# Optimization experiments

Measured on AMD Instinct MI355X. Metric: run time of the kernel, lower is better.

Reference implementation:

```python
import jax, jax.numpy as jnp
import numpy as np

B, L, D, H = 4, 2048, 1024, 16
DH = D // H  # 64
MASK_VALUE = -1000000.0
EPS = 1e-12


def setup_inputs() -> dict:
    key = jax.random.key(0)
    ks = jax.random.split(key, 7)
    s = 1.0 / np.sqrt(D)
    x = jax.random.normal(ks[0], (B, L, D), dtype=jnp.float32)
    Wq = jax.random.uniform(ks[1], (D, H * DH), jnp.float32, -s, s)
    Wk = jax.random.uniform(ks[2], (D, H * DH), jnp.float32, -s, s)
    Wv = jax.random.uniform(ks[3], (D, H * DH), jnp.float32, -s, s)
    Wo = jax.random.uniform(ks[4], (H * DH, D), jnp.float32, -s, s)
    gamma = jnp.ones((D,), jnp.float32)
    beta = jnp.zeros((D,), jnp.float32)
    # causal mask: True positions are masked (query m cannot attend to key n > m)
    attn_mask = jnp.triu(jnp.ones((L, L), dtype=bool), k=1)
    return {"x": x, "Wq": Wq, "Wk": Wk, "Wv": Wv, "Wo": Wo,
            "gamma": gamma, "beta": beta, "attn_mask": attn_mask}


def _layernorm(y, gamma, beta):
    mu = jnp.mean(y, axis=-1, keepdims=True)
    var = jnp.mean(jnp.square(y - mu), axis=-1, keepdims=True)
    return (y - mu) * jax.lax.rsqrt(var + EPS) * gamma + beta


def reference(x, Wq, Wk, Wv, Wo, gamma, beta, attn_mask):
    scale = 1.0 / np.sqrt(DH)
    # projections, reshape to heads: B L (H D) -> B H L D
    q = (x @ Wq).reshape(B, L, H, DH).transpose(0, 2, 1, 3)
    k = (x @ Wk).reshape(B, L, H, DH).transpose(0, 2, 1, 3)
    v = (x @ Wv).reshape(B, L, H, DH).transpose(0, 2, 1, 3)
    scores = jnp.einsum('bhmd,bhnd->bhmn', q, k) * scale
    scores = jnp.where(attn_mask, MASK_VALUE, scores)
    probs = jax.nn.softmax(scores, axis=-1)
    z = jnp.einsum('bhmn,bhnd->bhmd', probs, v)
    z = z.transpose(0, 2, 1, 3).reshape(B, L, H * DH)
    out = jax.nn.relu(z @ Wo)
    return _layernorm(out + x, gamma, beta)
```

## Files before the change

### kernel.cpp

```cpp
#include <hip/hip_runtime.h>
#include <math.h>

#define B_ 4
#define L_ 2048
#define D_ 1024
#define H_ 16
#define DH_ 64
#define QKV_N 3072

typedef unsigned short ushort_t;
typedef unsigned int uint_t;
using bf16x8 = __attribute__((ext_vector_type(8))) short;
using f32x4  = __attribute__((ext_vector_type(4))) float;

__device__ __forceinline__ ushort_t f2bf(float f) {
    union { float f; unsigned int u; } v; v.f = f;
    unsigned int u = v.u;
    unsigned int rnd = ((u >> 16) & 1u) + 0x7fffu;
    return (ushort_t)((u + rnd) >> 16);
}

__device__ __forceinline__ float bf2f(ushort_t u) {
    union { unsigned int u; float f; } v;
    v.u = ((unsigned int)u) << 16;
    return v.f;
}

__device__ __forceinline__ void glds16(const void* g, void* l) {
    __builtin_amdgcn_global_load_lds(
        (const __attribute__((address_space(1))) unsigned int*)g,
        (__attribute__((address_space(3))) unsigned int*)l, 16, 0, 0);
}

__global__ __launch_bounds__(256) void prep(const float* __restrict__ Wq,
                                            const float* __restrict__ Wk,
                                            const float* __restrict__ Wv,
                                            const float* __restrict__ Wo,
                                            const float* __restrict__ x,
                                            ushort_t* __restrict__ wcat,
                                            ushort_t* __restrict__ wto,
                                            ushort_t* __restrict__ xb) {
    const int t = threadIdx.x;
    if (blockIdx.z == 4) {
        const int bid = blockIdx.y * 16 + blockIdx.x;
        const int base = bid * 32768 + t * 4;
        #pragma unroll
        for (int it = 0; it < 32; ++it) {
            float4 v = *(const float4*)(x + base + it * 1024);
            ushort4 o;
            o.x = f2bf(v.x); o.y = f2bf(v.y); o.z = f2bf(v.z); o.w = f2bf(v.w);
            *(ushort4*)(xb + base + it * 1024) = o;
        }
        return;
    }
    __shared__ ushort_t tile[64][65];
    const int widx = blockIdx.z;
    const float* W = (widx == 0) ? Wq : (widx == 1) ? Wk : (widx == 2) ? Wv : Wo;
    ushort_t* dst = (widx < 3) ? (wcat + (size_t)widx * 1024 * 1024) : wto;
    const int j = t & 63, i0 = t >> 6;
    const int kbase = blockIdx.y * 64, nbase = blockIdx.x * 64;
    #pragma unroll
    for (int it = 0; it < 16; ++it) {
        int i = it * 4 + i0;
        tile[i][j] = f2bf(W[(size_t)(kbase + i) * 1024 + nbase + j]);
    }
    __syncthreads();
    #pragma unroll
    for (int it = 0; it < 16; ++it) {
        int nn = it * 4 + i0;
        dst[(size_t)(nbase + nn) * 1024 + kbase + j] = tile[j][nn];
    }
}

__global__ __launch_bounds__(256) void gemm_mfma(const ushort_t* __restrict__ A,
                                                 const ushort_t* __restrict__ Wt,
                                                 ushort_t* __restrict__ Cbf,
                                                 const ushort_t* __restrict__ resid,
                                                 int M, int N, int K, int fuse) {
    __shared__ ushort_t As[128 * 64];
    __shared__ ushort_t Bs[128 * 64];
    const int t = threadIdx.x;
    const int w = t >> 6, ln = t & 63;
    const int l15 = ln & 15, quad = ln >> 4;
    const int bm = blockIdx.y * 128, bn = blockIdx.x * 128;
    const int wm = (w & 1) * 64, wn = (w >> 1) * 64;

    const ushort_t* Ap[4];
    const ushort_t* Bp[4];
    #pragma unroll
    for (int j = 0; j < 4; ++j) {
        const int i = t + j * 256;
        const int r = i >> 3;
        const int qg = (i & 7) ^ (r & 7);
        Ap[j] = A  + (size_t)(bm + r) * K + qg * 8;
        Bp[j] = Wt + (size_t)(bn + r) * K + qg * 8;
    }

    f32x4 acc[4][4] = {};

    for (int k0 = 0; k0 < K; k0 += 64) {
        __syncthreads();
        #pragma unroll
        for (int j = 0; j < 4; ++j) {
            glds16(Ap[j] + k0, &As[(t + j * 256) * 8]);
            glds16(Bp[j] + k0, &Bs[(t + j * 256) * 8]);
        }
        __syncthreads();

        #pragma unroll
        for (int kw = 0; kw < 2; ++kw) {
            bf16x8 af[4], bfr[4];
            #pragma unroll
            for (int im = 0; im < 4; ++im) {
                int row = wm + im * 16 + l15;
                int phys = (kw * 4 + quad) ^ (row & 7);
                af[im] = *(const bf16x8*)&As[row * 64 + phys * 8];
            }
            #pragma unroll
            for (int in = 0; in < 4; ++in) {
                int row = wn + in * 16 + l15;
                int phys = (kw * 4 + quad) ^ (row & 7);
                bfr[in] = *(const bf16x8*)&Bs[row * 64 + phys * 8];
            }
            #pragma unroll
            for (int im = 0; im < 4; ++im)
                #pragma unroll
                for (int in = 0; in < 4; ++in)
                    acc[im][in] = __builtin_amdgcn_mfma_f32_16x16x32_bf16(
                        af[im], bfr[in], acc[im][in], 0, 0, 0);
        }
    }

    #pragma unroll
    for (int im = 0; im < 4; ++im) {
        #pragma unroll
        for (int in = 0; in < 4; ++in) {
            #pragma unroll
            for (int reg = 0; reg < 4; ++reg) {
                int row = bm + wm + im * 16 + quad * 4 + reg;
                int col = bn + wn + in * 16 + l15;
                size_t idx = (size_t)row * N + col;
                float v = acc[im][in][reg];
                if (fuse) v = fmaxf(v, 0.f) + bf2f(resid[idx]);
                Cbf[idx] = f2bf(v);
            }
        }
    }
}

__global__ __launch_bounds__(256) void transv(const ushort_t* __restrict__ qkv,
                                              ushort_t* __restrict__ Vt) {
    __shared__ ushort_t tile[64][65];
    const int t = threadIdx.x, j = t & 63, i0 = t >> 6;
    const int tt = blockIdx.x, h = blockIdx.y, b = blockIdx.z;
    #pragma unroll
    for (int it = 0; it < 16; ++it) {
        int i = it * 4 + i0;
        tile[i][j] = qkv[(size_t)(b * L_ + tt * 64 + i) * QKV_N + 2048 + h * DH_ + j];
    }
    __syncthreads();
    const int pj = (j & 3) * 16 + (j >> 2);
    #pragma unroll
    for (int it = 0; it < 16; ++it) {
        int d = it * 4 + i0;
        Vt[(size_t)((b * H_ + h) * DH_ + d) * L_ + tt * 64 + j] = tile[pj][d];
    }
}

__global__ __launch_bounds__(256) void attn_mfma(const ushort_t* __restrict__ qkv,
                                                 const ushort_t* __restrict__ Vt,
                                                 ushort_t* __restrict__ Zb) {
    __shared__ ushort_t Ks[128 * 64];
    __shared__ ushort_t Vs[64 * 128];
    __shared__ ushort_t Ps[4][32 * 72];
    const int t = threadIdx.x, w = t >> 6, ln = t & 63;
    const int l15 = ln & 15, quad = ln >> 4;
    const int bh = blockIdx.x;
    const int b = bh >> 4, h = bh & 15;
    const int Qt = 15 - blockIdx.y;

    bf16x8 ones;
    #pragma unroll
    for (int i = 0; i < 8; ++i) ones[i] = (short)0x3f80;

    int kkey[4], kq[4], vd[4], vcq[4];
    #pragma unroll
    for (int j = 0; j < 4; ++j) {
        int i = t + j * 256;
        kkey[j] = i >> 3;
        kq[j]   = (i & 7) ^ (kkey[j] & 7);
        vd[j]   = i >> 4;
        int cqp = i & 15;
        vcq[j]  = (cqp & 8) | ((cqp & 7) ^ (vd[j] & 7));
    }
    const ushort_t* Kgb = qkv + 1024 + (size_t)b * L_ * QKV_N + h * DH_;
    const ushort_t* Vgb = Vt + (size_t)((b * H_ + h) * DH_) * L_;

    bf16x8 qf[2][2];
    #pragma unroll
    for (int mt = 0; mt < 2; ++mt) {
        const ushort_t* qrow =
            qkv + (size_t)(b * L_ + Qt * 128 + w * 32 + mt * 16 + l15) * QKV_N + h * DH_;
        qf[mt][0] = *(const bf16x8*)(qrow + quad * 8);
        qf[mt][1] = *(const bf16x8*)(qrow + 32 + quad * 8);
    }

    f32x4 acc_o[2][4] = {};
    f32x4 l_acc[2] = {};

    const float c2 = 0.18033688f;

    for (int kt = 0; kt <= Qt; ++kt) {
        __syncthreads();
        #pragma unroll
        for (int j = 0; j < 4; ++j) {
            glds16(Kgb + (size_t)(kt * 128 + kkey[j]) * QKV_N + kq[j] * 8,
                   &Ks[(t + j * 256) * 8]);
            glds16(Vgb + (size_t)vd[j] * L_ + kt * 128 + vcq[j] * 8,
                   &Vs[(t + j * 256) * 8]);
        }
        __syncthreads();

        const bool masked = (kt == Qt);

        #pragma unroll
        for (int ph = 0; ph < 2; ++ph) {
            if (masked && ph && w < 2) continue;

            f32x4 acc_s[2][4] = {};
            #pragma unroll
            for (int in = 0; in < 4; ++in) {
                const int key = ph * 64 + in * 16 + l15;
                #pragma unroll
                for (int ks = 0; ks < 2; ++ks) {
                    int phys = (ks * 4 + quad) ^ (key & 7);
                    bf16x8 kf = *(const bf16x8*)&Ks[key * 64 + phys * 8];
                    acc_s[0][in] = __builtin_amdgcn_mfma_f32_16x16x32_bf16(
                        qf[0][ks], kf, acc_s[0][in], 0, 0, 0);
                    acc_s[1][in] = __builtin_amdgcn_mfma_f32_16x16x32_bf16(
                        qf[1][ks], kf, acc_s[1][in], 0, 0, 0);
                }
            }

            #pragma unroll
            for (int mt = 0; mt < 2; ++mt) {
                #pragma unroll
                for (int reg = 0; reg < 4; ++reg) {
                    const int row = mt * 16 + quad * 4 + reg;
                    float pv[4];
                    #pragma unroll
                    for (int in = 0; in < 4; ++in) {
                        float s2 = fmaf(acc_s[mt][in][reg], c2, -2.0f);
                        if (masked) {
                            int col = kt * 128 + ph * 64 + in * 16 + l15;
                            int qg  = Qt * 128 + w * 32 + row;
                            s2 = (col > qg) ? -100000.0f : s2;
                        }
                        pv[in] = __builtin_amdgcn_exp2f(s2);
                    }
                    uint_t u01 = __builtin_amdgcn_perm(
                        __float_as_uint(pv[1]), __float_as_uint(pv[0]), 0x07060302u);
                    uint_t u23 = __builtin_amdgcn_perm(
                        __float_as_uint(pv[3]), __float_as_uint(pv[2]), 0x07060302u);
                    uint2* dst = (uint2*)&Ps[w][row * 72 + l15 * 4];
                    *dst = make_uint2(u01, u23);
                }
            }

            #pragma unroll
            for (int ks = 0; ks < 2; ++ks) {
                bf16x8 pf0 = *(const bf16x8*)&Ps[w][(l15) * 72 + ks * 32 + quad * 8];
                bf16x8 pf1 = *(const bf16x8*)&Ps[w][(16 + l15) * 72 + ks * 32 + quad * 8];
                #pragma unroll
                for (int in = 0; in < 4; ++in) {
                    const int d = in * 16 + l15;
                    int physv = ph * 8 + (((ks * 4 + quad) ^ (d & 7)));
                    bf16x8 vf = *(const bf16x8*)&Vs[d * 128 + physv * 8];
                    acc_o[0][in] = __builtin_amdgcn_mfma_f32_16x16x32_bf16(
                        vf, pf0, acc_o[0][in], 0, 0, 0);
                    acc_o[1][in] = __builtin_amdgcn_mfma_f32_16x16x32_bf16(
                        vf, pf1, acc_o[1][in], 0, 0, 0);
                }
                l_acc[0] = __builtin_amdgcn_mfma_f32_16x16x32_bf16(ones, pf0, l_acc[0], 0, 0, 0);
                l_acc[1] = __builtin_amdgcn_mfma_f32_16x16x32_bf16(ones, pf1, l_acc[1], 0, 0, 0);
            }
        }
    }

    #pragma unroll
    for (int mt = 0; mt < 2; ++mt) {
        const float inv = 1.0f / l_acc[mt][0];
        const int row = b * L_ + Qt * 128 + w * 32 + mt * 16 + l15;
        #pragma unroll
        for (int in = 0; in < 4; ++in) {
            const int dbase = h * DH_ + in * 16 + quad * 4;
            f32x4 a = acc_o[mt][in];
            ushort4 o;
            o.x = f2bf(a[0] * inv); o.y = f2bf(a[1] * inv);
            o.z = f2bf(a[2] * inv); o.w = f2bf(a[3] * inv);
            *(ushort4*)(Zb + (size_t)row * D_ + dbase) = o;
        }
    }
}

__global__ __launch_bounds__(64) void ln_kernel(const ushort_t* __restrict__ Y,
                                                const float* __restrict__ gamma,
                                                const float* __restrict__ beta,
                                                float* __restrict__ out) {
    const int row = blockIdx.x;
    const int t = threadIdx.x;
    const ushort_t* y = Y + (size_t)row * D_;

    float v[16];
    #pragma unroll
    for (int s = 0; s < 4; ++s) {
        ushort4 u = *(const ushort4*)(y + s * 256 + t * 4);
        v[s * 4 + 0] = bf2f(u.x);
        v[s * 4 + 1] = bf2f(u.y);
        v[s * 4 + 2] = bf2f(u.z);
        v[s * 4 + 3] = bf2f(u.w);
    }

    float sum = 0.f;
    #pragma unroll
    for (int i = 0; i < 16; ++i) sum += v[i];
    #pragma unroll
    for (int k = 1; k < 64; k <<= 1) sum += __shfl_xor(sum, k, 64);
    const float mu = sum * (1.f / (float)D_);

    float var = 0.f;
    #pragma unroll
    for (int i = 0; i < 16; ++i) {
        float d = v[i] - mu;
        var += d * d;
    }
    #pragma unroll
    for (int k = 1; k < 64; k <<= 1) var += __shfl_xor(var, k, 64);
    const float rstd = rsqrtf(var * (1.f / (float)D_) + 1e-12f);

    #pragma unroll
    for (int s = 0; s < 4; ++s) {
        const int col = s * 256 + t * 4;
        float4 g  = *(const float4*)(gamma + col);
        float4 bb = *(const float4*)(beta + col);
        float4 o;
        o.x = (v[s * 4 + 0] - mu) * rstd * g.x + bb.x;
        o.y = (v[s * 4 + 1] - mu) * rstd * g.y + bb.y;
        o.z = (v[s * 4 + 2] - mu) * rstd * g.z + bb.z;
        o.w = (v[s * 4 + 3] - mu) * rstd * g.w + bb.w;
        *(float4*)(out + (size_t)row * D_ + col) = o;
    }
}

extern "C" void kernel_launch(void* const* d_in, const int* in_sizes, int n_in,
                              void* d_out, int out_size, void* d_ws, size_t ws_size,
                              hipStream_t stream) {
    const float* x     = (const float*)d_in[0];
    const float* Wq    = (const float*)d_in[1];
    const float* Wk    = (const float*)d_in[2];
    const float* Wv    = (const float*)d_in[3];
    const float* Wo    = (const float*)d_in[4];
    const float* gamma = (const float*)d_in[5];
    const float* beta  = (const float*)d_in[6];
    float* out = (float*)d_out;

    char* ws = (char*)d_ws;
    ushort_t* x_bf = (ushort_t*)(ws);
    ushort_t* wcat = (ushort_t*)(ws + (16u  << 20));
    ushort_t* wto  = (ushort_t*)(ws + (22u  << 20));
    ushort_t* qkv  = (ushort_t*)(ws + (24u  << 20));
    ushort_t* vt   = (ushort_t*)(ws + (72u  << 20));
    ushort_t* z_bf = (ushort_t*)(ws + (88u  << 20));
    ushort_t* y_bf = (ushort_t*)(ws + (104u << 20));

    const int M = B_ * L_;

    prep<<<dim3(16, 16, 5), 256, 0, stream>>>(Wq, Wk, Wv, Wo, x, wcat, wto, x_bf);

    gemm_mfma<<<dim3(QKV_N / 128, M / 128), 256, 0, stream>>>(
        x_bf, wcat, qkv, nullptr, M, QKV_N, D_, 0);

    transv<<<dim3(L_ / 64, H_, B_), 256, 0, stream>>>(qkv, vt);

    attn_mfma<<<dim3(B_ * H_, 16), 256, 0, stream>>>(qkv, vt, z_bf);

    gemm_mfma<<<dim3(D_ / 128, M / 128), 256, 0, stream>>>(
        z_bf, wto, y_bf, x_bf, M, D_, D_, 1);

    ln_kernel<<<M, 64, 0, stream>>>(y_bf, gamma, beta, out);
}
```

Before: 288.3 us.

## Fuse V transpose into QKV GEMM epilogue and enlarge attention query tile

The QKV GEMM epilogue now writes V directly into the transposed, permuted layout the attention kernel expects, so the separate transpose kernel and its extra global memory round trip are gone. The attention kernel processes 256 queries per block, 64 per wave, so each K/V tile loaded into shared memory is reused across more queries. Causal skipping and masking are now decided per wave at 64-key granularity. In exchange, the V stores are scattered 2-byte writes, the attention grid is halved, and register pressure rises with four query subtiles per wave.

New measurement: 313.9 us. 8.9% more time.

```diff
diff --git a/kernel.cpp b/kernel.cpp
--- a/kernel.cpp
+++ b/kernel.cpp
@@ -76,6 +76,7 @@
                                                  const ushort_t* __restrict__ Wt,
                                                  ushort_t* __restrict__ Cbf,
                                                  const ushort_t* __restrict__ resid,
+                                                 ushort_t* __restrict__ vt,
                                                  int M, int N, int K, int fuse) {
     __shared__ ushort_t As[128 * 64];
     __shared__ ushort_t Bs[128 * 64];
@@ -131,39 +132,41 @@
         }
     }
 
-    #pragma unroll
-    for (int im = 0; im < 4; ++im) {
-        #pragma unroll
-        for (int in = 0; in < 4; ++in) {
-            #pragma unroll
-            for (int reg = 0; reg < 4; ++reg) {
-                int row = bm + wm + im * 16 + quad * 4 + reg;
-                int col = bn + wn + in * 16 + l15;
-                size_t idx = (size_t)row * N + col;
-                float v = acc[im][in][reg];
-                if (fuse) v = fmaxf(v, 0.f) + bf2f(resid[idx]);
-                Cbf[idx] = f2bf(v);
-            }
-        }
-    }
-}
-
-__global__ __launch_bounds__(256) void transv(const ushort_t* __restrict__ qkv,
-                                              ushort_t* __restrict__ Vt) {
-    __shared__ ushort_t tile[64][65];
-    const int t = threadIdx.x, j = t & 63, i0 = t >> 6;
-    const int tt = blockIdx.x, h = blockIdx.y, b = blockIdx.z;
-    #pragma unroll
-    for (int it = 0; it < 16; ++it) {
-        int i = it * 4 + i0;
-        tile[i][j] = qkv[(size_t)(b * L_ + tt * 64 + i) * QKV_N + 2048 + h * DH_ + j];
-    }
-    __syncthreads();
-    const int pj = (j & 3) * 16 + (j >> 2);
-    #pragma unroll
-    for (int it = 0; it < 16; ++it) {
-        int d = it * 4 + i0;
-        Vt[(size_t)((b * H_ + h) * DH_ + d) * L_ + tt * 64 + j] = tile[pj][d];
+    if (vt && bn >= 2048) {
+        #pragma unroll
+        for (int im = 0; im < 4; ++im) {
+            #pragma unroll
+            for (int in = 0; in < 4; ++in) {
+                #pragma unroll
+                for (int reg = 0; reg < 4; ++reg) {
+                    int row = bm + wm + im * 16 + quad * 4 + reg;
+                    int col = bn + wn + in * 16 + l15 - 2048;
+                    int bb = row >> 11, tok = row & 2047;
+                    int h = col >> 6, d = col & 63;
+                    int tg = tok & 63;
+                    int sc = (tg & 15) * 4 + (tg >> 4);
+                    size_t addr = ((size_t)((bb * 16 + h) * 64 + d) << 11)
+                                + (tok & ~63) + sc;
+                    vt[addr] = f2bf(acc[im][in][reg]);
+                }
+            }
+        }
+    } else {
+        #pragma unroll
+        for (int im = 0; im < 4; ++im) {
+            #pragma unroll
+            for (int in = 0; in < 4; ++in) {
+                #pragma unroll
+                for (int reg = 0; reg < 4; ++reg) {
+                    int row = bm + wm + im * 16 + quad * 4 + reg;
+                    int col = bn + wn + in * 16 + l15;
+                    size_t idx = (size_t)row * N + col;
+                    float v = acc[im][in][reg];
+                    if (fuse) v = fmaxf(v, 0.f) + bf2f(resid[idx]);
+                    Cbf[idx] = f2bf(v);
+                }
+            }
+        }
     }
 }
 
@@ -172,12 +175,12 @@
                                                  ushort_t* __restrict__ Zb) {
     __shared__ ushort_t Ks[128 * 64];
     __shared__ ushort_t Vs[64 * 128];
-    __shared__ ushort_t Ps[4][32 * 72];
+    __shared__ ushort_t Ps[4][64 * 72];
     const int t = threadIdx.x, w = t >> 6, ln = t & 63;
     const int l15 = ln & 15, quad = ln >> 4;
     const int bh = blockIdx.x;
     const int b = bh >> 4, h = bh & 15;
-    const int Qt = 15 - blockIdx.y;
+    const int Qt = 7 - blockIdx.y;
 
     bf16x8 ones;
     #pragma unroll
@@ -196,21 +199,23 @@
     const ushort_t* Kgb = qkv + 1024 + (size_t)b * L_ * QKV_N + h * DH_;
     const ushort_t* Vgb = Vt + (size_t)((b * H_ + h) * DH_) * L_;
 
-    bf16x8 qf[2][2];
-    #pragma unroll
-    for (int mt = 0; mt < 2; ++mt) {
+    bf16x8 qf[4][2];
+    #pragma unroll
+    for (int mt = 0; mt < 4; ++mt) {
         const ushort_t* qrow =
-            qkv + (size_t)(b * L_ + Qt * 128 + w * 32 + mt * 16 + l15) * QKV_N + h * DH_;
+            qkv + (size_t)(b * L_ + Qt * 256 + w * 64 + mt * 16 + l15) * QKV_N + h * DH_;
         qf[mt][0] = *(const bf16x8*)(qrow + quad * 8);
         qf[mt][1] = *(const bf16x8*)(qrow + 32 + quad * 8);
     }
 
-    f32x4 acc_o[2][4] = {};
-    f32x4 l_acc[2] = {};
+    f32x4 acc_o[4][4] = {};
+    f32x4 l_acc[4] = {};
 
     const float c2 = 0.18033688f;
-
-    for (int kt = 0; kt <= Qt; ++kt) {
+    const int wq0 = Qt * 256 + w * 64;
+    const int ktmax = 2 * Qt + 1;
+
+    for (int kt = 0; kt <= ktmax; ++kt) {
         __syncthreads();
         #pragma unroll
         for (int j = 0; j < 4; ++j) {
@@ -221,39 +226,36 @@
         }
         __syncthreads();
 
-        const bool masked = (kt == Qt);
-
         #pragma unroll
         for (int ph = 0; ph < 2; ++ph) {
-            if (masked && ph && w < 2) continue;
-
-            f32x4 acc_s[2][4] = {};
-            #pragma unroll
-            for (int in = 0; in < 4; ++in) {
-                const int key = ph * 64 + in * 16 + l15;
-                #pragma unroll
-                for (int ks = 0; ks < 2; ++ks) {
-                    int phys = (ks * 4 + quad) ^ (key & 7);
-                    bf16x8 kf = *(const bf16x8*)&Ks[key * 64 + phys * 8];
-                    acc_s[0][in] = __builtin_amdgcn_mfma_f32_16x16x32_bf16(
-                        qf[0][ks], kf, acc_s[0][in], 0, 0, 0);
-                    acc_s[1][in] = __builtin_amdgcn_mfma_f32_16x16x32_bf16(
-                        qf[1][ks], kf, acc_s[1][in], 0, 0, 0);
-                }
-            }
-
-            #pragma unroll
-            for (int mt = 0; mt < 2; ++mt) {
+            const int keylo = kt * 128 + ph * 64;
+            if (keylo > wq0 + 63) continue;
+            const bool needMask = (keylo + 63 > wq0);
+
+            #pragma unroll
+            for (int mt = 0; mt < 4; ++mt) {
+                f32x4 accs[4] = {};
+                #pragma unroll
+                for (int in = 0; in < 4; ++in) {
+                    const int key = ph * 64 + in * 16 + l15;
+                    #pragma unroll
+                    for (int ks = 0; ks < 2; ++ks) {
+                        int phys = (ks * 4 + quad) ^ (key & 7);
+                        bf16x8 kf = *(const bf16x8*)&Ks[key * 64 + phys * 8];
+                        accs[in] = __builtin_amdgcn_mfma_f32_16x16x32_bf16(
+                            qf[mt][ks], kf, accs[in], 0, 0, 0);
+                    }
+                }
                 #pragma unroll
                 for (int reg = 0; reg < 4; ++reg) {
                     const int row = mt * 16 + quad * 4 + reg;
                     float pv[4];
                     #pragma unroll
                     for (int in = 0; in < 4; ++in) {
-                        float s2 = fmaf(acc_s[mt][in][reg], c2, -2.0f);
-                        if (masked) {
-                            int col = kt * 128 + ph * 64 + in * 16 + l15;
-                            int qg  = Qt * 128 + w * 32 + row;
+                        float s2 = fmaf(accs[in][reg], c2, -2.0f);
+                        if (needMask) {
+                            int col = keylo + in * 16 + l15;
+                            int qg  = wq0 + row;
                             s2 = (col > qg) ? -100000.0f : s2;
                         }
                         pv[in] = __builtin_amdgcn_exp2f(s2);
@@ -269,28 +271,32 @@
 
             #pragma unroll
             for (int ks = 0; ks < 2; ++ks) {
-                bf16x8 pf0 = *(const bf16x8*)&Ps[w][(l15) * 72 + ks * 32 + quad * 8];
-                bf16x8 pf1 = *(const bf16x8*)&Ps[w][(16 + l15) * 72 + ks * 32 + quad * 8];
+                bf16x8 pf[4];
+                #pragma unroll
+                for (int mt = 0; mt < 4; ++mt)
+                    pf[mt] = *(const bf16x8*)&Ps[w][(mt * 16 + l15) * 72 + ks * 32 + quad * 8];
                 #pragma unroll
                 for (int in = 0; in < 4; ++in) {
                     const int d = in * 16 + l15;
                     int physv = ph * 8 + (((ks * 4 + quad) ^ (d & 7)));
                     bf16x8 vf = *(const bf16x8*)&Vs[d * 128 + physv * 8];
-                    acc_o[0][in] = __builtin_amdgcn_mfma_f32_16x16x32_bf16(
-                        vf, pf0, acc_o[0][in], 0, 0, 0);
-                    acc_o[1][in] = __builtin_amdgcn_mfma_f32_16x16x32_bf16(
-                        vf, pf1, acc_o[1][in], 0, 0, 0);
-                }
-                l_acc[0] = __builtin_amdgcn_mfma_f32_16x16x32_bf16(ones, pf0, l_acc[0], 0, 0, 0);
-                l_acc[1] = __builtin_amdgcn_mfma_f32_16x16x32_bf16(ones, pf1, l_acc[1], 0, 0, 0);
-            }
-        }
-    }
-
-    #pragma unroll
-    for (int mt = 0; mt < 2; ++mt) {
+                    #pragma unroll
+                    for (int mt = 0; mt < 4; ++mt)
+                        acc_o[mt][in] = __builtin_amdgcn_mfma_f32_16x16x32_bf16(
+                            vf, pf[mt], acc_o[mt][in], 0, 0, 0);
+                }
+                #pragma unroll
+                for (int mt = 0; mt < 4; ++mt)
+                    l_acc[mt] = __builtin_amdgcn_mfma_f32_16x16x32_bf16(
+                        ones, pf[mt], l_acc[mt], 0, 0, 0);
+            }
+        }
+    }
+
+    #pragma unroll
+    for (int mt = 0; mt < 4; ++mt) {
         const float inv = 1.0f / l_acc[mt][0];
-        const int row = b * L_ + Qt * 128 + w * 32 + mt * 16 + l15;
+        const int row = b * L_ + Qt * 256 + w * 64 + mt * 16 + l15;
         #pragma unroll
         for (int in = 0; in < 4; ++in) {
             const int dbase = h * DH_ + in * 16 + quad * 4;
@@ -378,14 +384,12 @@
     prep<<<dim3(16, 16, 5), 256, 0, stream>>>(Wq, Wk, Wv, Wo, x, wcat, wto, x_bf);
 
     gemm_mfma<<<dim3(QKV_N / 128, M / 128), 256, 0, stream>>>(
-        x_bf, wcat, qkv, nullptr, M, QKV_N, D_, 0);
-
-    transv<<<dim3(L_ / 64, H_, B_), 256, 0, stream>>>(qkv, vt);
-
-    attn_mfma<<<dim3(B_ * H_, 16), 256, 0, stream>>>(qkv, vt, z_bf);
+        x_bf, wcat, qkv, nullptr, vt, M, QKV_N, D_, 0);
+
+    attn_mfma<<<dim3(B_ * H_, 8), 256, 0, stream>>>(qkv, vt, z_bf);
 
     gemm_mfma<<<dim3(D_ / 128, M / 128), 256, 0, stream>>>(
-        z_bf, wto, y_bf, x_bf, M, D_, D_, 1);
+        z_bf, wto, y_bf, x_bf, nullptr, M, D_, D_, 1);
 
     ln_kernel<<<M, 64, 0, stream>>>(y_bf, gamma, beta, out);
 }
```
